# Optimization experiments

Hardware: AMD Instinct MI355X
Metric: run time of the kernel (lower is better)

## Reference

```python
import jax, jax.numpy as jnp
import numpy as np
import math

B_GRAPHS = 256
L_NODES = 64
N_NODES = B_GRAPHS * L_NODES
N_EDGES = N_NODES * 4
HEADS = 8
D_INNER = 512
N_DAGS = 1
DIAMETER = 64


def setup_inputs() -> dict:
    key = jax.random.key(0)
    ks = jax.random.split(key, 8)
    x = jax.random.normal(ks[0], (N_NODES, D_INNER), jnp.float32)
    B = jax.random.normal(ks[1], (N_NODES, D_INNER), jnp.float32)
    C = jax.random.normal(ks[2], (N_NODES, D_INNER), jnp.float32)
    dt = jax.random.normal(ks[3], (N_NODES, N_DAGS * HEADS * 2), jnp.float32)
    dt_edge = jax.random.normal(ks[4], (N_EDGES, N_DAGS * HEADS), jnp.float32)
    # DAG edges: within each graph, src_local < dst_local (gap 1..7) -> strictly upper triangular
    u = jax.random.randint(ks[5], (N_EDGES,), 0, L_NODES - 1)
    gap = jax.random.randint(ks[6], (N_EDGES,), 1, 8)
    v = jnp.minimum(u + gap, L_NODES - 1)
    graph = jnp.arange(N_EDGES) // (N_EDGES // B_GRAPHS)
    edge_index = jnp.stack([graph * L_NODES + u, graph * L_NODES + v]).astype(jnp.int32)
    data_batch = (jnp.arange(N_NODES) // L_NODES).astype(jnp.int32)
    dag_masks = jnp.ones((N_DAGS, N_EDGES), jnp.float32)
    # dt_bias init as in module __init__ (inverse softplus of dt in [1e-3, 1e-1])
    rng = np.random.default_rng(0)
    dtv = np.exp(rng.uniform(size=(HEADS,)) * (math.log(0.1) - math.log(0.001)) + math.log(0.001))
    dtv = np.clip(dtv, 1e-4, None)
    dt_bias = jnp.asarray(dtv + np.log(-np.expm1(-dtv)), jnp.float32)
    D = jnp.ones((HEADS,), jnp.float32)
    return dict(x=x, B=B, C=C, dt=dt, dt_edge=dt_edge, dt_bias=dt_bias, D=D,
                dag_masks=dag_masks, edge_index=edge_index, data_batch=data_batch,
                diameter=DIAMETER)


def _repeated_squaring_inverse(A, diam):
    # (I - A)^{-1} = prod_k (I + A^{2^k}) for nilpotent A; O(log diam) matmuls
    j = 2 ** int(math.ceil(math.log2(diam)))
    I = jnp.eye(A.shape[-1], dtype=A.dtype)
    last = A
    M = I + A
    for _ in range(2, int(math.log2(j)) + 1):
        last = last @ last
        M = M @ (I + last)
    return M


def reference(x, B, C, dt, dt_edge, dt_bias, D, dag_masks, edge_index, data_batch, diameter):
    N, din = x.shape
    g, E = dag_masks.shape
    n = dt_bias.shape[0]
    b = int(data_batch[-1]) + 1
    l = N // b  # equal-size graphs -> dense batching is a reshape, mask all-True
    h = din // n
    src, dst = edge_index[0], edge_index[1]

    # dt_node: (N, g*n*c) -> (c, g, n, N); softplus(dt + bias)
    c = dt.shape[1] // (g * n)
    dtn = dt.reshape(N, g, n, c).transpose(3, 1, 2, 0)
    dtn = jax.nn.softplus(dtn + dt_bias[None, None, :, None])
    dte = dt_edge.reshape(E, g, n).transpose(1, 2, 0)  # (g,n,E)
    dte = jax.nn.softplus(dte + dt_bias[None, :, None])

    dt_s, dt_t = dtn[0], dtn[1]
    dt_sum = (dt_s[:, :, src] + dt_t[:, :, dst] + dte) / np.sqrt(3.0)  # (g,n,E)
    dt_exp = jnp.exp(-dt_sum)
    msk = dag_masks[:, None, :]
    dt_sum = dt_sum * msk
    dt_exp = dt_exp * msk

    # dense adjacency with per-edge attrs; note 'b l1 l2 (g n) -> b g n l2 l1' transpose
    b_e = src // l
    sl = src % l
    dl = dst % l
    attr = dt_exp.transpose(2, 0, 1).reshape(E, g * n)
    adj = jnp.zeros((b, l, l, g * n), x.dtype).at[b_e, sl, dl].add(attr)
    A = adj.reshape(b, l, l, g, n).transpose(0, 3, 4, 2, 1)  # (b,g,n,l,l)

    # normalize_mat: sqrt outer product of in-degree counts, clamped at 1
    ec = jnp.zeros((g, N), x.dtype).at[:, dst].add(dag_masks)
    ec_dense = ec.T.reshape(b, l, g)
    outer = jnp.sqrt(jnp.einsum('blg,btg->bglt', ec_dense, ec_dense))
    outer = jnp.where(outer < 1.0, 1.0, outer)
    A = A / outer[:, :, None]

    dnorm = jnp.zeros((g, n, N), x.dtype).at[:, :, dst].add(dt_sum)
    dnorm = dnorm.transpose(2, 0, 1).reshape(b, l, g, n).transpose(0, 2, 3, 1)  # (b,g,n,l)

    A2 = A.reshape(b, g * n, l, l).astype(jnp.float32)
    L = _repeated_squaring_inverse(A2, int(diameter))
    L = L.reshape(b, g, n, l, l) * dnorm[..., None]

    x4 = x.reshape(b, l, n, h).transpose(0, 2, 1, 3)  # (b,n,l,h)
    B3 = B.reshape(b, l, -1)
    C3 = C.reshape(b, l, -1)
    # y = einsum(C,L,B,x) with B/C broadcast over (g,n): fold C.B^T into L
    CB = jnp.einsum('bld,btd->blt', C3, B3)
    M = L * CB[:, None, None]
    y = jnp.einsum('bgnlt,bnth->bgnlh', M, x4)
    y = y + x4[:, None] * D[None, None, :, None, None]
    y = y.transpose(0, 3, 1, 2, 4).reshape(N, g, n * h)  # b g n l h -> (N, g, n*h)
    y = y.sum(axis=1) / np.sqrt(g)
    return y
```

## Files before the change

kernel.cpp:

```cpp
#include <hip/hip_runtime.h>
#include <math.h>

#define NGRAPH 256
#define HEADS  8
#define DIN    512
#define EPG    256
#define NEDGE  65536
#define LOG2E 1.44269504088896341f
#define LN2   0.69314718055994531f

typedef short bf16x8 __attribute__((ext_vector_type(8)));
typedef float f32x4 __attribute__((ext_vector_type(4)));

__device__ __forceinline__ float softplusf(float v) {
    if (v > 20.f) return v;
    float t = exp2f(v * LOG2E);
    return LN2 * log2f(1.f + t);
}
__device__ __forceinline__ unsigned short f2bf(float f) {
    union { float f; unsigned u; } c; c.f = f;
    unsigned r = c.u + 0x7fffu + ((c.u >> 16) & 1u);
    return (unsigned short)(r >> 16);
}
__device__ __forceinline__ float bf2f(unsigned short h) {
    union { float f; unsigned u; } c; c.u = ((unsigned)h) << 16;
    return c.f;
}
__device__ __forceinline__ int swz_idx(int row, int t) {
    int g = ((t >> 3) ^ (row ^ (row >> 3))) & 7;
    return (row << 6) | (g << 3) | (t & 7);
}
__device__ __forceinline__ void loadsplit(const float* p, bf16x8& hi, bf16x8& lo) {
    float4 u = *(const float4*)p;
    float4 v = *(const float4*)(p + 4);
    float vv[8] = {u.x, u.y, u.z, u.w, v.x, v.y, v.z, v.w};
    #pragma unroll
    for (int j = 0; j < 8; ++j) {
        union { float f; unsigned q; } c; c.f = vv[j];
        unsigned hb = c.q & 0xffff0000u;
        hi[j] = (short)(unsigned short)(hb >> 16);
        union { float f; unsigned q; } d; d.q = hb;
        union { float f; unsigned q; } e2; e2.f = vv[j] - d.f;
        lo[j] = (short)(unsigned short)(e2.q >> 16);
    }
}

__global__ __launch_bounds__(512, 2) void dag_fused_v2(
        const float* __restrict__ x,
        const float* __restrict__ Bm,
        const float* __restrict__ Cm,
        const float* __restrict__ dt,
        const float* __restrict__ dt_edge,
        const float* __restrict__ dt_bias,
        const float* __restrict__ Dp,
        const float* __restrict__ dag_masks,
        const int* __restrict__ edge_index,
        float* __restrict__ out) {
    __shared__ unsigned short CBsh[64 * 68];
    __shared__ __align__(16) unsigned short Xt[HEADS][4096];
    __shared__ __align__(16) unsigned short Wl[HEADS][4096];
    __shared__ float Ab[HEADS][448];
    __shared__ float dts[HEADS][64];
    __shared__ float dtt[HEADS][64];
    __shared__ float dnsh[HEADS][64];
    __shared__ float ecsh[64];

    const int b = blockIdx.x;
    const int tid = threadIdx.x;
    const int w = tid >> 6;
    const int lane = tid & 63;
    const int lm = lane & 15;
    const int quad = lane >> 4;
    const float bias = dt_bias[w];

    {
        float2 dv = *(const float2*)(dt + ((size_t)(b * 64 + lane)) * 16 + w * 2);
        dts[w][lane] = softplusf(dv.x + bias);
        dtt[w][lane] = softplusf(dv.y + bias);
        dnsh[w][lane] = 0.f;
        #pragma unroll
        for (int s = 0; s < 7; ++s) Ab[w][lane * 7 + s] = 0.f;
        if (w == 0) ecsh[lane] = 0.f;
    }

    {
        const int mi = w >> 1;
        const int ni0 = (w & 1) * 2;
        const float* Cr = Cm + ((size_t)(b * 64 + mi * 16 + lm)) * DIN + quad * 8;
        const float* B0 = Bm + ((size_t)(b * 64 + ni0 * 16 + lm)) * DIN + quad * 8;
        const float* B1 = B0 + (size_t)16 * DIN;
        f32x4 acc0 = {0.f, 0.f, 0.f, 0.f};
        f32x4 acc1 = {0.f, 0.f, 0.f, 0.f};
        #pragma unroll 4
        for (int ks = 0; ks < 16; ++ks) {
            bf16x8 ah, al, b0h, b0l, b1h, b1l;
            loadsplit(Cr + ks * 32, ah, al);
            loadsplit(B0 + ks * 32, b0h, b0l);
            loadsplit(B1 + ks * 32, b1h, b1l);
            acc0 = __builtin_amdgcn_mfma_f32_16x16x32_bf16(ah, b0h, acc0, 0, 0, 0);
            acc0 = __builtin_amdgcn_mfma_f32_16x16x32_bf16(ah, b0l, acc0, 0, 0, 0);
            acc0 = __builtin_amdgcn_mfma_f32_16x16x32_bf16(al, b0h, acc0, 0, 0, 0);
            acc1 = __builtin_amdgcn_mfma_f32_16x16x32_bf16(ah, b1h, acc1, 0, 0, 0);
            acc1 = __builtin_amdgcn_mfma_f32_16x16x32_bf16(ah, b1l, acc1, 0, 0, 0);
            acc1 = __builtin_amdgcn_mfma_f32_16x16x32_bf16(al, b1h, acc1, 0, 0, 0);
        }
        #pragma unroll
        for (int r = 0; r < 4; ++r) {
            int row = mi * 16 + quad * 4 + r;
            CBsh[row * 68 + ni0 * 16 + lm] = f2bf(acc0[r]);
            CBsh[row * 68 + (ni0 + 1) * 16 + lm] = f2bf(acc1[r]);
        }
    }

    {
        const float* xg = x + (size_t)b * 64 * DIN + w * 64;
        #pragma unroll
        for (int r = 0; r < 4; ++r) {
            int t0 = quad * 4 + r * 16;
            int e0 = lm * 4;
            float4 v0 = *(const float4*)(xg + (size_t)(t0 + 0) * DIN + e0);
            float4 v1 = *(const float4*)(xg + (size_t)(t0 + 1) * DIN + e0);
            float4 v2 = *(const float4*)(xg + (size_t)(t0 + 2) * DIN + e0);
            float4 v3 = *(const float4*)(xg + (size_t)(t0 + 3) * DIN + e0);
            float a0[4] = {v0.x, v0.y, v0.z, v0.w};
            float a1[4] = {v1.x, v1.y, v1.z, v1.w};
            float a2[4] = {v2.x, v2.y, v2.z, v2.w};
            float a3[4] = {v3.x, v3.y, v3.z, v3.w};
            #pragma unroll
            for (int k = 0; k < 4; ++k) {
                unsigned long long pk =
                      (unsigned long long)f2bf(a0[k])
                    | ((unsigned long long)f2bf(a1[k]) << 16)
                    | ((unsigned long long)f2bf(a2[k]) << 32)
                    | ((unsigned long long)f2bf(a3[k]) << 48);
                *(unsigned long long*)(&Xt[w][swz_idx(e0 + k, t0)]) = pk;
            }
        }
    }

    {
        #pragma unroll
        for (int eo = 0; eo < 4; ++eo) {
            int e = b * EPG + eo * 64 + lane;
            int sl = edge_index[e] & 63;
            int dl = edge_index[NEDGE + e] & 63;
            float mk = dag_masks[e];
            float de = softplusf(dt_edge[(size_t)e * HEADS + w] + bias);
            float dsum = (dts[w][sl] + dtt[w][dl] + de) * 0.57735026918962576451f;
            float dexp = exp2f(-dsum * LOG2E);
            atomicAdd(&Ab[w][dl * 7 + (dl - sl - 1)], dexp * mk);
            atomicAdd(&dnsh[w][dl], dsum * mk);
            if (w == 0) atomicAdd(&ecsh[dl], mk);
        }
    }

    __syncthreads();

    {
        float eci = ecsh[lane];
        #pragma unroll
        for (int s = 0; s < 7; ++s) {
            int src = lane - 1 - s;
            if (src >= 0) {
                float p = eci * ecsh[src];
                float f = fminf(1.f, rsqrtf(p));
                Ab[w][lane * 7 + s] *= f;
            }
        }
    }

    {
        const int j = lane;
        const float Dh = Dp[w];
        float mwin[7] = {0.f, 0.f, 0.f, 0.f, 0.f, 0.f, 0.f};
        float cab[7];
        #pragma unroll
        for (int s = 0; s < 7; ++s) cab[s] = Ab[w][s];
        float cbv = bf2f(CBsh[j]);
        float dnv = dnsh[w][0];
        for (int i = 0; i < 64; ++i) {
            float nab[7], ncb = 0.f, ndn = 0.f;
            if (i < 63) {
                #pragma unroll
                for (int s = 0; s < 7; ++s) nab[s] = Ab[w][(i + 1) * 7 + s];
                ncb = bf2f(CBsh[(i + 1) * 68 + j]);
                ndn = dnsh[w][i + 1];
            } else {
                #pragma unroll
                for (int s = 0; s < 7; ++s) nab[s] = 0.f;
            }
            float diag = (j == i) ? 1.f : 0.f;
            float t0 = fmaf(cab[0], mwin[0], fmaf(cab[1], mwin[1], diag));
            float t1 = fmaf(cab[2], mwin[2], fmaf(cab[3], mwin[3], cab[4] * mwin[4]));
            float t2 = fmaf(cab[5], mwin[5], cab[6] * mwin[6]);
            float mi_ = t0 + (t1 + t2);
            float wv = mi_ * cbv * dnv;
            if (j == i) wv += Dh;
            Wl[w][swz_idx(i, j)] = f2bf(wv);
            #pragma unroll
            for (int s = 6; s > 0; --s) mwin[s] = mwin[s - 1];
            mwin[0] = mi_;
            #pragma unroll
            for (int s = 0; s < 7; ++s) cab[s] = nab[s];
            cbv = ncb;
            dnv = ndn;
        }
    }

    {
        bf16x8 af[4][2];
        #pragma unroll
        for (int mi = 0; mi < 4; ++mi) {
            int row0 = mi * 16 + lm;
            af[mi][0] = *(const bf16x8*)(&Wl[w][swz_idx(row0, quad * 8)]);
            af[mi][1] = *(const bf16x8*)(&Wl[w][swz_idx(row0, 32 + quad * 8)]);
        }
        float* og = out + (size_t)b * 64 * DIN + w * 64;
        #pragma unroll
        for (int eb = 0; eb < 4; ++eb) {
            int er = eb * 16 + lm;
            bf16x8 b0 = *(const bf16x8*)(&Xt[w][swz_idx(er, quad * 8)]);
            bf16x8 b1 = *(const bf16x8*)(&Xt[w][swz_idx(er, 32 + quad * 8)]);
            #pragma unroll
            for (int mi = 0; mi < 4; ++mi) {
                f32x4 acc = {0.f, 0.f, 0.f, 0.f};
                acc = __builtin_amdgcn_mfma_f32_16x16x32_bf16(af[mi][0], b0, acc, 0, 0, 0);
                acc = __builtin_amdgcn_mfma_f32_16x16x32_bf16(af[mi][1], b1, acc, 0, 0, 0);
                #pragma unroll
                for (int r = 0; r < 4; ++r) {
                    int row = mi * 16 + quad * 4 + r;
                    og[(size_t)row * DIN + eb * 16 + lm] = acc[r];
                }
            }
        }
    }
}

extern "C" void kernel_launch(void* const* d_in, const int* in_sizes, int n_in,
                              void* d_out, int out_size, void* d_ws, size_t ws_size,
                              hipStream_t stream) {
    (void)in_sizes; (void)n_in; (void)out_size; (void)d_ws; (void)ws_size;
    dag_fused_v2<<<dim3(NGRAPH), dim3(512), 0, stream>>>(
        (const float*)d_in[0],
        (const float*)d_in[1],
        (const float*)d_in[2],
        (const float*)d_in[3],
        (const float*)d_in[4],
        (const float*)d_in[5],
        (const float*)d_in[6],
        (const float*)d_in[7],
        (const int*)d_in[8],
        (float*)d_out);
}
```

Measured before the change: 165.8 us.

## Stage B and C chunks cooperatively in double-buffered LDS for CB product

```diff
diff --git a/kernel.cpp b/kernel.cpp
--- a/kernel.cpp
+++ b/kernel.cpp
@@ -30,22 +30,45 @@
     int g = ((t >> 3) ^ (row ^ (row >> 3))) & 7;
     return (row << 6) | (g << 3) | (t & 7);
 }
-__device__ __forceinline__ void loadsplit(const float* p, bf16x8& hi, bf16x8& lo) {
-    float4 u = *(const float4*)p;
-    float4 v = *(const float4*)(p + 4);
-    float vv[8] = {u.x, u.y, u.z, u.w, v.x, v.y, v.z, v.w};
+__device__ __forceinline__ void split1(float f, unsigned short& hi, unsigned short& lo) {
+    union { float f; unsigned q; } c; c.f = f;
+    unsigned hb = c.q & 0xffff0000u;
+    hi = (unsigned short)(hb >> 16);
+    union { float f; unsigned q; } d; d.q = hb;
+    union { float f; unsigned q; } e2; e2.f = f - d.f;
+    lo = (unsigned short)(e2.q >> 16);
+}
+
+__device__ __forceinline__ void stage_chunk(int c, unsigned short* buf,
+                                            const float* __restrict__ Cm,
+                                            const float* __restrict__ Bm,
+                                            int b, int tid) {
     #pragma unroll
-    for (int j = 0; j < 8; ++j) {
-        union { float f; unsigned q; } c; c.f = vv[j];
-        unsigned hb = c.q & 0xffff0000u;
-        hi[j] = (short)(unsigned short)(hb >> 16);
-        union { float f; unsigned q; } d; d.q = hb;
-        union { float f; unsigned q; } e2; e2.f = vv[j] - d.f;
-        lo[j] = (short)(unsigned short)(e2.q >> 16);
-    }
-}
-
-__global__ __launch_bounds__(512, 2) void dag_fused_v2(
+    for (int i = 0; i < 4; ++i) {
+        int u = tid * 4 + i;
+        int mat = u >> 10;
+        int rem = u & 1023;
+        int row = rem >> 4;
+        int col4 = (rem & 15) << 2;
+        const float* src = (mat ? Bm : Cm) + ((size_t)(b * 64 + row)) * DIN + c * 64 + col4;
+        float4 v = *(const float4*)src;
+        float a[4] = {v.x, v.y, v.z, v.w};
+        unsigned long long hp = 0, lp = 0;
+        #pragma unroll
+        for (int k = 0; k < 4; ++k) {
+            unsigned short h, l;
+            split1(a[k], h, l);
+            hp |= ((unsigned long long)h) << (16 * k);
+            lp |= ((unsigned long long)l) << (16 * k);
+        }
+        int idx = swz_idx(row, col4);
+        unsigned short* thi = buf + (mat ? 8192 : 0);
+        *(unsigned long long*)(thi + idx) = hp;
+        *(unsigned long long*)(thi + 4096 + idx) = lp;
+    }
+}
+
+__global__ __launch_bounds__(512, 2) void dag_fused_v3(
         const float* __restrict__ x,
         const float* __restrict__ Bm,
         const float* __restrict__ Cm,
@@ -56,9 +79,9 @@
         const float* __restrict__ dag_masks,
         const int* __restrict__ edge_index,
         float* __restrict__ out) {
-    __shared__ unsigned short CBsh[64 * 68];
+    __shared__ __align__(16) unsigned short WS[32768];
     __shared__ __align__(16) unsigned short Xt[HEADS][4096];
-    __shared__ __align__(16) unsigned short Wl[HEADS][4096];
+    __shared__ __align__(16) unsigned short CBsh[4096];
     __shared__ float Ab[HEADS][448];
     __shared__ float dts[HEADS][64];
     __shared__ float dtt[HEADS][64];
@@ -84,31 +107,18 @@
     }
 
     {
-        const int mi = w >> 1;
-        const int ni0 = (w & 1) * 2;
-        const float* Cr = Cm + ((size_t)(b * 64 + mi * 16 + lm)) * DIN + quad * 8;
-        const float* B0 = Bm + ((size_t)(b * 64 + ni0 * 16 + lm)) * DIN + quad * 8;
-        const float* B1 = B0 + (size_t)16 * DIN;
-        f32x4 acc0 = {0.f, 0.f, 0.f, 0.f};
-        f32x4 acc1 = {0.f, 0.f, 0.f, 0.f};
-        #pragma unroll 4
-        for (int ks = 0; ks < 16; ++ks) {
-            bf16x8 ah, al, b0h, b0l, b1h, b1l;
-            loadsplit(Cr + ks * 32, ah, al);
-            loadsplit(B0 + ks * 32, b0h, b0l);
-            loadsplit(B1 + ks * 32, b1h, b1l);
-            acc0 = __builtin_amdgcn_mfma_f32_16x16x32_bf16(ah, b0h, acc0, 0, 0, 0);
-            acc0 = __builtin_amdgcn_mfma_f32_16x16x32_bf16(ah, b0l, acc0, 0, 0, 0);
-            acc0 = __builtin_amdgcn_mfma_f32_16x16x32_bf16(al, b0h, acc0, 0, 0, 0);
-            acc1 = __builtin_amdgcn_mfma_f32_16x16x32_bf16(ah, b1h, acc1, 0, 0, 0);
-            acc1 = __builtin_amdgcn_mfma_f32_16x16x32_bf16(ah, b1l, acc1, 0, 0, 0);
-            acc1 = __builtin_amdgcn_mfma_f32_16x16x32_bf16(al, b1h, acc1, 0, 0, 0);
-        }
-        #pragma unroll
-        for (int r = 0; r < 4; ++r) {
-            int row = mi * 16 + quad * 4 + r;
-            CBsh[row * 68 + ni0 * 16 + lm] = f2bf(acc0[r]);
-            CBsh[row * 68 + (ni0 + 1) * 16 + lm] = f2bf(acc1[r]);
+        #pragma unroll
+        for (int eo = 0; eo < 4; ++eo) {
+            int e = b * EPG + eo * 64 + lane;
+            int sl = edge_index[e] & 63;
+            int dl = edge_index[NEDGE + e] & 63;
+            float mk = dag_masks[e];
+            float de = softplusf(dt_edge[(size_t)e * HEADS + w] + bias);
+            float dsum = (dts[w][sl] + dtt[w][dl] + de) * 0.57735026918962576451f;
+            float dexp = exp2f(-dsum * LOG2E);
+            atomicAdd(&Ab[w][dl * 7 + (dl - sl - 1)], dexp * mk);
+            atomicAdd(&dnsh[w][dl], dsum * mk);
+            if (w == 0) atomicAdd(&ecsh[dl], mk);
         }
     }
 
@@ -138,22 +148,38 @@
         }
     }
 
-    {
-        #pragma unroll
-        for (int eo = 0; eo < 4; ++eo) {
-            int e = b * EPG + eo * 64 + lane;
-            int sl = edge_index[e] & 63;
-            int dl = edge_index[NEDGE + e] & 63;
-            float mk = dag_masks[e];
-            float de = softplusf(dt_edge[(size_t)e * HEADS + w] + bias);
-            float dsum = (dts[w][sl] + dtt[w][dl] + de) * 0.57735026918962576451f;
-            float dexp = exp2f(-dsum * LOG2E);
-            atomicAdd(&Ab[w][dl * 7 + (dl - sl - 1)], dexp * mk);
-            atomicAdd(&dnsh[w][dl], dsum * mk);
-            if (w == 0) atomicAdd(&ecsh[dl], mk);
-        }
-    }
-
+    const int mi = w >> 1;
+    const int ni0 = (w & 1) * 2;
+    f32x4 acc0 = {0.f, 0.f, 0.f, 0.f};
+    f32x4 acc1 = {0.f, 0.f, 0.f, 0.f};
+    stage_chunk(0, WS, Cm, Bm, b, tid);
+    for (int c = 0; c < 8; ++c) {
+        __syncthreads();
+        if (c < 7) stage_chunk(c + 1, WS + ((c + 1) & 1) * 16384, Cm, Bm, b, tid);
+        const unsigned short* p = WS + (c & 1) * 16384;
+        #pragma unroll
+        for (int ks = 0; ks < 2; ++ks) {
+            int kl = ks * 32 + quad * 8;
+            bf16x8 ah  = *(const bf16x8*)(p +         swz_idx(mi * 16 + lm, kl));
+            bf16x8 al  = *(const bf16x8*)(p +  4096 + swz_idx(mi * 16 + lm, kl));
+            bf16x8 b0h = *(const bf16x8*)(p +  8192 + swz_idx(ni0 * 16 + lm, kl));
+            bf16x8 b0l = *(const bf16x8*)(p + 12288 + swz_idx(ni0 * 16 + lm, kl));
+            bf16x8 b1h = *(const bf16x8*)(p +  8192 + swz_idx((ni0 + 1) * 16 + lm, kl));
+            bf16x8 b1l = *(const bf16x8*)(p + 12288 + swz_idx((ni0 + 1) * 16 + lm, kl));
+            acc0 = __builtin_amdgcn_mfma_f32_16x16x32_bf16(ah, b0h, acc0, 0, 0, 0);
+            acc0 = __builtin_amdgcn_mfma_f32_16x16x32_bf16(ah, b0l, acc0, 0, 0, 0);
+            acc0 = __builtin_amdgcn_mfma_f32_16x16x32_bf16(al, b0h, acc0, 0, 0, 0);
+            acc1 = __builtin_amdgcn_mfma_f32_16x16x32_bf16(ah, b1h, acc1, 0, 0, 0);
+            acc1 = __builtin_amdgcn_mfma_f32_16x16x32_bf16(ah, b1l, acc1, 0, 0, 0);
+            acc1 = __builtin_amdgcn_mfma_f32_16x16x32_bf16(al, b1h, acc1, 0, 0, 0);
+        }
+    }
+    #pragma unroll
+    for (int r = 0; r < 4; ++r) {
+        int row = mi * 16 + quad * 4 + r;
+        CBsh[row * 64 + ni0 * 16 + lm] = f2bf(acc0[r]);
+        CBsh[row * 64 + (ni0 + 1) * 16 + lm] = f2bf(acc1[r]);
+    }
     __syncthreads();
 
     {
@@ -169,6 +195,7 @@
         }
     }
 
+    unsigned short* Wlw = WS + w * 4096;
     {
         const int j = lane;
         const float Dh = Dp[w];
@@ -183,7 +210,7 @@
             if (i < 63) {
                 #pragma unroll
                 for (int s = 0; s < 7; ++s) nab[s] = Ab[w][(i + 1) * 7 + s];
-                ncb = bf2f(CBsh[(i + 1) * 68 + j]);
+                ncb = bf2f(CBsh[(i + 1) * 64 + j]);
                 ndn = dnsh[w][i + 1];
             } else {
                 #pragma unroll
@@ -196,7 +223,7 @@
             float mi_ = t0 + (t1 + t2);
             float wv = mi_ * cbv * dnv;
             if (j == i) wv += Dh;
-            Wl[w][swz_idx(i, j)] = f2bf(wv);
+            Wlw[swz_idx(i, j)] = f2bf(wv);
             #pragma unroll
             for (int s = 6; s > 0; --s) mwin[s] = mwin[s - 1];
             mwin[0] = mi_;
@@ -208,29 +235,33 @@
     }
 
     {
-        bf16x8 af[4][2];
-        #pragma unroll
-        for (int mi = 0; mi < 4; ++mi) {
-            int row0 = mi * 16 + lm;
-            af[mi][0] = *(const bf16x8*)(&Wl[w][swz_idx(row0, quad * 8)]);
-            af[mi][1] = *(const bf16x8*)(&Wl[w][swz_idx(row0, 32 + quad * 8)]);
-        }
-        float* og = out + (size_t)b * 64 * DIN + w * 64;
+        bf16x8 bf[4][2];
         #pragma unroll
         for (int eb = 0; eb < 4; ++eb) {
             int er = eb * 16 + lm;
-            bf16x8 b0 = *(const bf16x8*)(&Xt[w][swz_idx(er, quad * 8)]);
-            bf16x8 b1 = *(const bf16x8*)(&Xt[w][swz_idx(er, 32 + quad * 8)]);
-            #pragma unroll
-            for (int mi = 0; mi < 4; ++mi) {
-                f32x4 acc = {0.f, 0.f, 0.f, 0.f};
-                acc = __builtin_amdgcn_mfma_f32_16x16x32_bf16(af[mi][0], b0, acc, 0, 0, 0);
-                acc = __builtin_amdgcn_mfma_f32_16x16x32_bf16(af[mi][1], b1, acc, 0, 0, 0);
+            bf[eb][0] = *(const bf16x8*)(&Xt[w][swz_idx(er, quad * 8)]);
+            bf[eb][1] = *(const bf16x8*)(&Xt[w][swz_idx(er, 32 + quad * 8)]);
+        }
+        float* og = out + (size_t)b * 64 * DIN + w * 64;
+        #pragma unroll
+        for (int m2 = 0; m2 < 4; ++m2) {
+            int row0 = m2 * 16 + lm;
+            bf16x8 a0 = *(const bf16x8*)(&Wlw[swz_idx(row0, quad * 8)]);
+            bf16x8 a1 = *(const bf16x8*)(&Wlw[swz_idx(row0, 32 + quad * 8)]);
+            f32x4 acc[4];
+            #pragma unroll
+            for (int eb = 0; eb < 4; ++eb) {
+                f32x4 z = {0.f, 0.f, 0.f, 0.f};
+                z = __builtin_amdgcn_mfma_f32_16x16x32_bf16(a0, bf[eb][0], z, 0, 0, 0);
+                z = __builtin_amdgcn_mfma_f32_16x16x32_bf16(a1, bf[eb][1], z, 0, 0, 0);
+                acc[eb] = z;
+            }
+            #pragma unroll
+            for (int r = 0; r < 4; ++r) {
+                int row = m2 * 16 + quad * 4 + r;
                 #pragma unroll
-                for (int r = 0; r < 4; ++r) {
-                    int row = mi * 16 + quad * 4 + r;
-                    og[(size_t)row * DIN + eb * 16 + lm] = acc[r];
-                }
+                for (int eb = 0; eb < 4; ++eb)
+                    og[(size_t)row * DIN + eb * 16 + lm] = acc[eb][r];
             }
         }
     }
@@ -240,7 +271,7 @@
                               void* d_out, int out_size, void* d_ws, size_t ws_size,
                               hipStream_t stream) {
     (void)in_sizes; (void)n_in; (void)out_size; (void)d_ws; (void)ws_size;
-    dag_fused_v2<<<dim3(NGRAPH), dim3(512), 0, stream>>>(
+    dag_fused_v3<<<dim3(NGRAPH), dim3(512), 0, stream>>>(
         (const float*)d_in[0],
         (const float*)d_in[1],
         (const float*)d_in[2],
```

After: 163.6 us. No clear change (-1.3%).

## Warp-specialize block: separate CB matmul warps from edge/scan warps, split output GEMM

Applied to the files above, without the earlier changes.

```diff
diff --git a/kernel.cpp b/kernel.cpp
--- a/kernel.cpp
+++ b/kernel.cpp
@@ -45,7 +45,7 @@
     }
 }
 
-__global__ __launch_bounds__(512, 2) void dag_fused_v2(
+__global__ __launch_bounds__(1024, 4) void dag_ws_v5(
         const float* __restrict__ x,
         const float* __restrict__ Bm,
         const float* __restrict__ Cm,
@@ -56,14 +56,13 @@
         const float* __restrict__ dag_masks,
         const int* __restrict__ edge_index,
         float* __restrict__ out) {
-    __shared__ unsigned short CBsh[64 * 68];
-    __shared__ __align__(16) unsigned short Xt[HEADS][4096];
-    __shared__ __align__(16) unsigned short Wl[HEADS][4096];
-    __shared__ float Ab[HEADS][448];
-    __shared__ float dts[HEADS][64];
-    __shared__ float dtt[HEADS][64];
-    __shared__ float dnsh[HEADS][64];
-    __shared__ float ecsh[64];
+    __shared__ __align__(16) unsigned short CBsh[4096];
+    __shared__ __align__(16) unsigned short Xt[8][4096];
+    __shared__ __align__(16) unsigned short Wl[8][4096];
+    __shared__ __align__(16) float Ab8[8][512];
+    __shared__ float dts[8][64];
+    __shared__ float dtt[8][64];
+    __shared__ float ecsh[8][64];
 
     const int b = blockIdx.x;
     const int tid = threadIdx.x;
@@ -71,21 +70,78 @@
     const int lane = tid & 63;
     const int lm = lane & 15;
     const int quad = lane >> 4;
-    const float bias = dt_bias[w];
-
-    {
-        float2 dv = *(const float2*)(dt + ((size_t)(b * 64 + lane)) * 16 + w * 2);
-        dts[w][lane] = softplusf(dv.x + bias);
-        dtt[w][lane] = softplusf(dv.y + bias);
-        dnsh[w][lane] = 0.f;
-        #pragma unroll
-        for (int s = 0; s < 7; ++s) Ab[w][lane * 7 + s] = 0.f;
-        if (w == 0) ecsh[lane] = 0.f;
-    }
-
-    {
-        const int mi = w >> 1;
-        const int ni0 = (w & 1) * 2;
+
+    if (w < 8) {
+        const float bias = dt_bias[w];
+        {
+            float2 dv = *(const float2*)(dt + ((size_t)(b * 64 + lane)) * 16 + w * 2);
+            dts[w][lane] = softplusf(dv.x + bias);
+            dtt[w][lane] = softplusf(dv.y + bias);
+            ecsh[w][lane] = 0.f;
+            float4 z = make_float4(0.f, 0.f, 0.f, 0.f);
+            *(float4*)(&Ab8[w][lane * 8]) = z;
+            *(float4*)(&Ab8[w][lane * 8 + 4]) = z;
+        }
+        {
+            #pragma unroll
+            for (int eo = 0; eo < 4; ++eo) {
+                int e = b * EPG + eo * 64 + lane;
+                int sl = edge_index[e] & 63;
+                int dl = edge_index[NEDGE + e] & 63;
+                float mk = dag_masks[e];
+                float de = softplusf(dt_edge[(size_t)e * HEADS + w] + bias);
+                float dsum = (dts[w][sl] + dtt[w][dl] + de) * 0.57735026918962576451f;
+                float dexp = exp2f(-dsum * LOG2E);
+                atomicAdd(&Ab8[w][dl * 8 + (dl - sl)], dexp * mk);
+                atomicAdd(&Ab8[w][dl * 8], dsum * mk);
+                atomicAdd(&ecsh[w][dl], mk);
+            }
+        }
+        {
+            const float* xg = x + (size_t)b * 64 * DIN + w * 64;
+            #pragma unroll
+            for (int r = 0; r < 4; ++r) {
+                int t0 = quad * 4 + r * 16;
+                int e0 = lm * 4;
+                float4 v0 = *(const float4*)(xg + (size_t)(t0 + 0) * DIN + e0);
+                float4 v1 = *(const float4*)(xg + (size_t)(t0 + 1) * DIN + e0);
+                float4 v2 = *(const float4*)(xg + (size_t)(t0 + 2) * DIN + e0);
+                float4 v3 = *(const float4*)(xg + (size_t)(t0 + 3) * DIN + e0);
+                float a0[4] = {v0.x, v0.y, v0.z, v0.w};
+                float a1[4] = {v1.x, v1.y, v1.z, v1.w};
+                float a2[4] = {v2.x, v2.y, v2.z, v2.w};
+                float a3[4] = {v3.x, v3.y, v3.z, v3.w};
+                #pragma unroll
+                for (int k = 0; k < 4; ++k) {
+                    unsigned long long pk =
+                          (unsigned long long)f2bf(a0[k])
+                        | ((unsigned long long)f2bf(a1[k]) << 16)
+                        | ((unsigned long long)f2bf(a2[k]) << 32)
+                        | ((unsigned long long)f2bf(a3[k]) << 48);
+                    *(unsigned long long*)(&Xt[w][swz_idx(e0 + k, t0)]) = pk;
+                }
+            }
+        }
+        {
+            float eci = ecsh[w][lane];
+            float4 a03 = *(const float4*)(&Ab8[w][lane * 8]);
+            float4 a47 = *(const float4*)(&Ab8[w][lane * 8 + 4]);
+            float sc[7];
+            #pragma unroll
+            for (int s = 0; s < 7; ++s) {
+                int src = lane - 1 - s;
+                float p = (src >= 0) ? eci * ecsh[w][src] : 1.f;
+                sc[s] = fminf(1.f, rsqrtf(p));
+            }
+            a03.y *= sc[0]; a03.z *= sc[1]; a03.w *= sc[2];
+            a47.x *= sc[3]; a47.y *= sc[4]; a47.z *= sc[5]; a47.w *= sc[6];
+            *(float4*)(&Ab8[w][lane * 8]) = a03;
+            *(float4*)(&Ab8[w][lane * 8 + 4]) = a47;
+        }
+    } else {
+        const int hw = w - 8;
+        const int mi = hw >> 1;
+        const int ni0 = (hw & 1) * 2;
         const float* Cr = Cm + ((size_t)(b * 64 + mi * 16 + lm)) * DIN + quad * 8;
         const float* B0 = Bm + ((size_t)(b * 64 + ni0 * 16 + lm)) * DIN + quad * 8;
         const float* B1 = B0 + (size_t)16 * DIN;
@@ -107,130 +163,79 @@
         #pragma unroll
         for (int r = 0; r < 4; ++r) {
             int row = mi * 16 + quad * 4 + r;
-            CBsh[row * 68 + ni0 * 16 + lm] = f2bf(acc0[r]);
-            CBsh[row * 68 + (ni0 + 1) * 16 + lm] = f2bf(acc1[r]);
-        }
-    }
-
-    {
-        const float* xg = x + (size_t)b * 64 * DIN + w * 64;
-        #pragma unroll
-        for (int r = 0; r < 4; ++r) {
-            int t0 = quad * 4 + r * 16;
-            int e0 = lm * 4;
-            float4 v0 = *(const float4*)(xg + (size_t)(t0 + 0) * DIN + e0);
-            float4 v1 = *(const float4*)(xg + (size_t)(t0 + 1) * DIN + e0);
-            float4 v2 = *(const float4*)(xg + (size_t)(t0 + 2) * DIN + e0);
-            float4 v3 = *(const float4*)(xg + (size_t)(t0 + 3) * DIN + e0);
-            float a0[4] = {v0.x, v0.y, v0.z, v0.w};
-            float a1[4] = {v1.x, v1.y, v1.z, v1.w};
-            float a2[4] = {v2.x, v2.y, v2.z, v2.w};
-            float a3[4] = {v3.x, v3.y, v3.z, v3.w};
-            #pragma unroll
-            for (int k = 0; k < 4; ++k) {
-                unsigned long long pk =
-                      (unsigned long long)f2bf(a0[k])
-                    | ((unsigned long long)f2bf(a1[k]) << 16)
-                    | ((unsigned long long)f2bf(a2[k]) << 32)
-                    | ((unsigned long long)f2bf(a3[k]) << 48);
-                *(unsigned long long*)(&Xt[w][swz_idx(e0 + k, t0)]) = pk;
-            }
-        }
-    }
-
-    {
-        #pragma unroll
-        for (int eo = 0; eo < 4; ++eo) {
-            int e = b * EPG + eo * 64 + lane;
-            int sl = edge_index[e] & 63;
-            int dl = edge_index[NEDGE + e] & 63;
-            float mk = dag_masks[e];
-            float de = softplusf(dt_edge[(size_t)e * HEADS + w] + bias);
-            float dsum = (dts[w][sl] + dtt[w][dl] + de) * 0.57735026918962576451f;
-            float dexp = exp2f(-dsum * LOG2E);
-            atomicAdd(&Ab[w][dl * 7 + (dl - sl - 1)], dexp * mk);
-            atomicAdd(&dnsh[w][dl], dsum * mk);
-            if (w == 0) atomicAdd(&ecsh[dl], mk);
+            CBsh[row * 64 + ni0 * 16 + lm] = f2bf(acc0[r]);
+            CBsh[row * 64 + (ni0 + 1) * 16 + lm] = f2bf(acc1[r]);
         }
     }
 
     __syncthreads();
 
-    {
-        float eci = ecsh[lane];
-        #pragma unroll
-        for (int s = 0; s < 7; ++s) {
-            int src = lane - 1 - s;
-            if (src >= 0) {
-                float p = eci * ecsh[src];
-                float f = fminf(1.f, rsqrtf(p));
-                Ab[w][lane * 7 + s] *= f;
-            }
-        }
-    }
-
-    {
+    if (w < 8) {
         const int j = lane;
         const float Dh = Dp[w];
         float mwin[7] = {0.f, 0.f, 0.f, 0.f, 0.f, 0.f, 0.f};
-        float cab[7];
-        #pragma unroll
-        for (int s = 0; s < 7; ++s) cab[s] = Ab[w][s];
+        float4 a03 = *(const float4*)(&Ab8[w][0]);
+        float4 a47 = *(const float4*)(&Ab8[w][4]);
         float cbv = bf2f(CBsh[j]);
-        float dnv = dnsh[w][0];
+        #pragma unroll 2
         for (int i = 0; i < 64; ++i) {
-            float nab[7], ncb = 0.f, ndn = 0.f;
+            float4 n03, n47;
+            float ncb = 0.f;
             if (i < 63) {
-                #pragma unroll
-                for (int s = 0; s < 7; ++s) nab[s] = Ab[w][(i + 1) * 7 + s];
-                ncb = bf2f(CBsh[(i + 1) * 68 + j]);
-                ndn = dnsh[w][i + 1];
+                n03 = *(const float4*)(&Ab8[w][(i + 1) * 8]);
+                n47 = *(const float4*)(&Ab8[w][(i + 1) * 8 + 4]);
+                ncb = bf2f(CBsh[(i + 1) * 64 + j]);
             } else {
-                #pragma unroll
-                for (int s = 0; s < 7; ++s) nab[s] = 0.f;
+                n03 = make_float4(0.f, 0.f, 0.f, 0.f);
+                n47 = n03;
             }
             float diag = (j == i) ? 1.f : 0.f;
-            float t0 = fmaf(cab[0], mwin[0], fmaf(cab[1], mwin[1], diag));
-            float t1 = fmaf(cab[2], mwin[2], fmaf(cab[3], mwin[3], cab[4] * mwin[4]));
-            float t2 = fmaf(cab[5], mwin[5], cab[6] * mwin[6]);
+            float t0 = fmaf(a03.y, mwin[0], fmaf(a03.z, mwin[1], diag));
+            float t1 = fmaf(a03.w, mwin[2], fmaf(a47.x, mwin[3], a47.y * mwin[4]));
+            float t2 = fmaf(a47.z, mwin[5], a47.w * mwin[6]);
             float mi_ = t0 + (t1 + t2);
-            float wv = mi_ * cbv * dnv;
+            float wv = mi_ * cbv * a03.x;
             if (j == i) wv += Dh;
             Wl[w][swz_idx(i, j)] = f2bf(wv);
             #pragma unroll
             for (int s = 6; s > 0; --s) mwin[s] = mwin[s - 1];
             mwin[0] = mi_;
-            #pragma unroll
-            for (int s = 0; s < 7; ++s) cab[s] = nab[s];
-            cbv = ncb;
-            dnv = ndn;
-        }
-    }
+            a03 = n03; a47 = n47; cbv = ncb;
+        }
+    }
+
+    __syncthreads();
 
     {
-        bf16x8 af[4][2];
-        #pragma unroll
-        for (int mi = 0; mi < 4; ++mi) {
-            int row0 = mi * 16 + lm;
-            af[mi][0] = *(const bf16x8*)(&Wl[w][swz_idx(row0, quad * 8)]);
-            af[mi][1] = *(const bf16x8*)(&Wl[w][swz_idx(row0, 32 + quad * 8)]);
-        }
-        float* og = out + (size_t)b * 64 * DIN + w * 64;
+        const int head = (w < 8) ? w : (w - 8);
+        const int m2base = (w < 8) ? 0 : 2;
+        bf16x8 bfr[4][2];
         #pragma unroll
         for (int eb = 0; eb < 4; ++eb) {
             int er = eb * 16 + lm;
-            bf16x8 b0 = *(const bf16x8*)(&Xt[w][swz_idx(er, quad * 8)]);
-            bf16x8 b1 = *(const bf16x8*)(&Xt[w][swz_idx(er, 32 + quad * 8)]);
-            #pragma unroll
-            for (int mi = 0; mi < 4; ++mi) {
-                f32x4 acc = {0.f, 0.f, 0.f, 0.f};
-                acc = __builtin_amdgcn_mfma_f32_16x16x32_bf16(af[mi][0], b0, acc, 0, 0, 0);
-                acc = __builtin_amdgcn_mfma_f32_16x16x32_bf16(af[mi][1], b1, acc, 0, 0, 0);
+            bfr[eb][0] = *(const bf16x8*)(&Xt[head][swz_idx(er, quad * 8)]);
+            bfr[eb][1] = *(const bf16x8*)(&Xt[head][swz_idx(er, 32 + quad * 8)]);
+        }
+        float* og = out + ((size_t)b * 64) * DIN + head * 64;
+        #pragma unroll
+        for (int m2o = 0; m2o < 2; ++m2o) {
+            int row0 = (m2base + m2o) * 16 + lm;
+            bf16x8 a0 = *(const bf16x8*)(&Wl[head][swz_idx(row0, quad * 8)]);
+            bf16x8 a1 = *(const bf16x8*)(&Wl[head][swz_idx(row0, 32 + quad * 8)]);
+            f32x4 acc[4];
+            #pragma unroll
+            for (int eb = 0; eb < 4; ++eb) {
+                f32x4 z = {0.f, 0.f, 0.f, 0.f};
+                z = __builtin_amdgcn_mfma_f32_16x16x32_bf16(a0, bfr[eb][0], z, 0, 0, 0);
+                z = __builtin_amdgcn_mfma_f32_16x16x32_bf16(a1, bfr[eb][1], z, 0, 0, 0);
+                acc[eb] = z;
+            }
+            #pragma unroll
+            for (int r = 0; r < 4; ++r) {
+                int row = (m2base + m2o) * 16 + quad * 4 + r;
                 #pragma unroll
-                for (int r = 0; r < 4; ++r) {
-                    int row = mi * 16 + quad * 4 + r;
-                    og[(size_t)row * DIN + eb * 16 + lm] = acc[r];
-                }
+                for (int eb = 0; eb < 4; ++eb)
+                    og[(size_t)row * DIN + eb * 16 + lm] = acc[eb][r];
             }
         }
     }
@@ -240,7 +245,7 @@
                               void* d_out, int out_size, void* d_ws, size_t ws_size,
                               hipStream_t stream) {
     (void)in_sizes; (void)n_in; (void)out_size; (void)d_ws; (void)ws_size;
-    dag_fused_v2<<<dim3(NGRAPH), dim3(512), 0, stream>>>(
+    dag_ws_v5<<<dim3(NGRAPH), dim3(1024), 0, stream>>>(
         (const float*)d_in[0],
         (const float*)d_in[1],
         (const float*)d_in[2],
```

Result: slower. 176.2 us (+6.3%).
